# Optimization experiments

Hardware: AMD Instinct MI355X
Metric: run time of the kernel (lower is better)

The kernel has to match this reference:

```python
import jax, jax.numpy as jnp
import numpy as np

RADIUS = 0.1
NSAMPLE = 32


def _ball_query(radius, nsample, xyz, new_xyz):
    # xyz: (B,N,3), new_xyz: (B,npoint,3) -> idx (B,npoint,nsample) int32
    # Faithful to the CUDA ball_query: take the first nsample in-radius indices
    # (in ascending point order); pad with the first found index.
    N = xyz.shape[1]
    d2 = jnp.sum((new_xyz[:, :, None, :] - xyz[:, None, :, :]) ** 2, axis=-1)  # (B,np,N)
    mask = d2 < radius * radius
    key_arr = jnp.where(mask, jnp.arange(N, dtype=jnp.int32), jnp.int32(N))
    idx = jnp.sort(key_arr, axis=-1)[..., :nsample]  # (B,np,ns)
    first = idx[..., :1]
    idx = jnp.where(idx == N, first, idx)
    idx = jnp.where(idx == N, 0, idx)  # empty-ball fallback (matches zero-init buffer)
    return idx


def _group(features, idx):
    # features (B,C,N), idx (B,np,ns) -> (B,C,np,ns)
    return jax.vmap(lambda f, i: f[:, i])(features, idx)


def _forward(xyz, new_xyz):
    idx = jax.lax.stop_gradient(_ball_query(RADIUS, NSAMPLE, xyz, new_xyz))
    xyz_t = jnp.transpose(xyz, (0, 2, 1))                 # (B,3,N)
    g = _group(xyz_t, idx)                                # (B,3,np,ns) grouped_xyz
    c = jnp.transpose(new_xyz, (0, 2, 1))[..., None]      # (B,3,np,1)  new_xyz_reshaped

    # pairwise distances within each group
    diff = g[..., :, None] - g[..., None, :]              # (B,3,np,ns,ns)
    dis = jnp.sqrt(jnp.sum(diff * diff, axis=1))          # (B,np,ns,ns)
    mean_dis = jnp.mean(dis, axis=3)                      # (B,np,ns)
    tip_idx = jnp.argmax(mean_dis, axis=2)                # (B,np)
    tip_pts = jnp.take_along_axis(g, tip_idx[:, None, :, None], axis=3)[..., 0]  # (B,3,np)

    cb = jnp.broadcast_to(c, g.shape)                     # (B,3,np,ns)
    gpv = jnp.cross(jnp.cross(cb, g, axis=1), cb, axis=1)
    gpv = gpv / jnp.linalg.norm(gpv, axis=1)[:, None]     # (B,3,np,ns)

    new_r = jnp.sqrt(jnp.sum(c * c, axis=1))              # (B,np,1)
    new_norm = c / (new_r[:, None] + 1e-8)                # (B,3,np,1)

    c3 = c[..., 0]                                        # (B,3,np)
    tpv = jnp.cross(jnp.cross(c3, tip_pts, axis=1), c3, axis=1)
    tpv = tpv / jnp.linalg.norm(tpv, axis=1)[:, None]     # (B,3,np)

    gcv = jnp.cross(gpv, jnp.broadcast_to(tpv[..., None], gpv.shape), axis=1)
    sinv = jnp.sum(gcv * new_norm, axis=1)                # (B,np,ns)

    dis_t = jnp.transpose(dis, (0, 2, 1, 3))              # (B,ns,np,ns)
    dis_sort = jnp.sort(dis_t, axis=1) * sinv[:, None]    # (B,ns,np,ns)
    grouped_r = jnp.sqrt(jnp.sum(g * g, axis=1))          # (B,np,ns)
    return jnp.concatenate([dis_sort, grouped_r[:, None]], axis=1)  # (B,ns+1,np,ns)


def setup_inputs() -> dict:
    key = jax.random.key(0)
    k1, k2 = jax.random.split(key)
    xyz = jax.random.uniform(k1, (4, 16384, 3), dtype=jnp.float32)
    new_xyz = jax.random.uniform(k2, (4, 2048, 3), dtype=jnp.float32)
    return {"xyz": xyz, "new_xyz": new_xyz}


def reference(xyz, new_xyz):
    return _forward(xyz, new_xyz)
```

## Files before the change

kernel.cpp:

```cpp
#include <hip/hip_runtime.h>


#define BB 4
#define NN 16384
#define MM 2048
#define NS 32
#define R2 0.01f
#define GZ 20
#define NCELL 2000
#define CPAD 2048
#define HCAP 128

#define WS_CUR_OFF (32 * 1024)
#define WS_CNT_OFF (64 * 1024)
#define WS_PTS_OFF (96 * 1024)
#define WS_NEED (WS_PTS_OFF + (size_t)BB * NN * 16)

__device__ __forceinline__ int cell_of(float x, float y, float z) {
    int ci = (int)(x * 10.0f); ci = ci < 0 ? 0 : (ci > 9 ? 9 : ci);
    int cj = (int)(y * 10.0f); cj = cj < 0 ? 0 : (cj > 9 ? 9 : cj);
    int ck = (int)(z * 20.0f); ck = ck < 0 ? 0 : (ck > 19 ? 19 : ck);
    return (ci * 10 + cj) * GZ + ck;
}

__global__ __launch_bounds__(256) void k_count(const float* __restrict__ xyz,
                                               int* __restrict__ cnt) {
    int i = blockIdx.x * 256 + threadIdx.x;
    int b = i >> 14;
    const float* p = xyz + (size_t)i * 3;
    atomicAdd(&cnt[b * CPAD + cell_of(p[0], p[1], p[2])], 1);
}

__global__ __launch_bounds__(1024) void k_scan(const int* __restrict__ cnt,
                                               int* __restrict__ off,
                                               int* __restrict__ cur) {
    __shared__ int wsum[16];
    const int b = blockIdx.x, t = threadIdx.x;
    const int lane = t & 63, wid = t >> 6;
    int v0 = cnt[b * CPAD + 2 * t];
    int v1 = cnt[b * CPAD + 2 * t + 1];
    int s = v0 + v1;
    int x = s;
    #pragma unroll
    for (int o = 1; o < 64; o <<= 1) {
        int u = __shfl_up(x, o);
        if (lane >= o) x += u;
    }
    if (lane == 63) wsum[wid] = x;
    __syncthreads();
    int pre = 0;
    #pragma unroll
    for (int i2 = 0; i2 < 16; ++i2) pre += (i2 < wid) ? wsum[i2] : 0;
    int incl = x + pre;
    int excl = incl - s;
    off[b * CPAD + 2 * t] = excl;
    off[b * CPAD + 2 * t + 1] = excl + v0;
    cur[b * CPAD + 2 * t] = excl;
    cur[b * CPAD + 2 * t + 1] = excl + v0;
}

__global__ __launch_bounds__(256) void k_scatter(const float* __restrict__ xyz,
                                                 int* __restrict__ cur,
                                                 float4* __restrict__ pts) {
    int i = blockIdx.x * 256 + threadIdx.x;
    int b = i >> 14;
    const float* p = xyz + (size_t)i * 3;
    float x = p[0], y = p[1], z = p[2];
    int pos = atomicAdd(&cur[b * CPAD + cell_of(x, y, z)], 1);
    pts[(size_t)b * NN + pos] = make_float4(x, y, z, __int_as_float(i & (NN - 1)));
}

__global__ __launch_bounds__(256) void qgr_grid_kernel(
    const float* __restrict__ xyz,
    const float* __restrict__ nxyz,
    const int* __restrict__ offi,
    const float4* __restrict__ pts,
    float* __restrict__ out) {

    __shared__ float4 s_hit[4][2][HCAP];
    __shared__ float4 s_sel[4][2][NS];

    const int lane = threadIdx.x & 63;
    const int w = threadIdx.x >> 6;
    const int sub = lane & 31;
    const int half = lane >> 5;
    const int q0 = blockIdx.x * 8 + w * 2;
    const int b = q0 >> 11;

    const float* xb = xyz + (size_t)b * NN * 3;
    const float* nq = nxyz + (size_t)q0 * 3;
    const float cx0 = nq[0], cy0 = nq[1], cz0 = nq[2];
    const float cx1 = nq[3], cy1 = nq[4], cz1 = nq[5];
    const unsigned long long lmask = (1ull << lane) - 1ull;

    const int* offb = offi + b * CPAD;
    const float4* ptsb = pts + (size_t)b * NN;

    int hits01[2];
    for (int tq = 0; tq < 2; ++tq) {
        const float ccx = tq ? cx1 : cx0;
        const float ccy = tq ? cy1 : cy0;
        const float ccz = tq ? cz1 : cz0;

        int ci0 = (int)(ccx * 10.0f); ci0 = ci0 < 0 ? 0 : (ci0 > 9 ? 9 : ci0);
        int cj0 = (int)(ccy * 10.0f); cj0 = cj0 < 0 ? 0 : (cj0 > 9 ? 9 : cj0);
        int ck0 = (int)(ccz * 20.0f); ck0 = ck0 < 0 ? 0 : (ck0 > 19 ? 19 : ck0);
        int zlo = ck0 > 2 ? ck0 - 2 : 0;
        int zhi = ck0 < 17 ? ck0 + 2 : 19;

        int rs[9], rl[9];
        #pragma unroll
        for (int r = 0; r < 9; ++r) { rs[r] = 0; rl[r] = 0; }
        int nr = 0;
        #pragma unroll
        for (int di = -1; di <= 1; ++di) {
            int ii = ci0 + di; if ((unsigned)ii > 9u) continue;
            #pragma unroll
            for (int dj = -1; dj <= 1; ++dj) {
                int jj = cj0 + dj; if ((unsigned)jj > 9u) continue;
                int base2 = (ii * 10 + jj) * GZ;
                int s0 = offb[base2 + zlo];
                int e0 = offb[base2 + zhi + 1];
                int len = e0 - s0;
                if (len > 0) { rs[nr] = s0; rl[nr] = len; ++nr; }
            }
        }

        float4 P[9];
        #pragma unroll
        for (int r = 0; r < 9; ++r) {
            int a = (lane < rl[r]) ? (rs[r] + lane) : 0;
            P[r] = ptsb[a];
        }

        int hits = 0;
        #pragma unroll
        for (int r = 0; r < 9; ++r) {
            float dx = __fsub_rn(ccx, P[r].x);
            float dy = __fsub_rn(ccy, P[r].y);
            float dz = __fsub_rn(ccz, P[r].z);
            float d2 = __fadd_rn(__fadd_rn(__fmul_rn(dx, dx), __fmul_rn(dy, dy)),
                                 __fmul_rn(dz, dz));
            bool hit = (lane < rl[r]) && (d2 < R2);
            unsigned long long bal = __ballot(hit);
            if (bal) {
                int rank = __popcll(bal & lmask);
                int slot = hits + rank;
                if (hit && slot < HCAP) s_hit[w][tq][slot] = P[r];
                hits += __popcll(bal);
            }
        }
        for (int r = 0; r < nr; ++r) {
            for (int t0 = 64; t0 < rl[r]; t0 += 64) {
                int t = t0 + lane;
                bool act = t < rl[r];
                float4 Q = ptsb[rs[r] + (act ? t : 0)];
                float dx = __fsub_rn(ccx, Q.x);
                float dy = __fsub_rn(ccy, Q.y);
                float dz = __fsub_rn(ccz, Q.z);
                float d2 = __fadd_rn(__fadd_rn(__fmul_rn(dx, dx), __fmul_rn(dy, dy)),
                                     __fmul_rn(dz, dz));
                bool hit = act && (d2 < R2);
                unsigned long long bal = __ballot(hit);
                if (bal) {
                    int rank = __popcll(bal & lmask);
                    int slot = hits + rank;
                    if (hit && slot < HCAP) s_hit[w][tq][slot] = Q;
                    hits += __popcll(bal);
                }
            }
        }
        hits01[tq] = hits;
    }

    const int hits = half ? hits01[1] : hits01[0];
    const int cap = hits < HCAP ? hits : HCAP;
    const float ccx = half ? cx1 : cx0;
    const float ccy = half ? cy1 : cy0;
    const float ccz = half ? cz1 : cz0;

    int key[4];
    #pragma unroll
    for (int r = 0; r < 4; ++r) {
        int e = r * 32 + sub;
        int idx_e = __float_as_int(s_hit[w][half][e].w);
        key[r] = (e < cap) ? ((idx_e << 8) | e) : 0x7fffffff;
    }

    #pragma unroll
    for (int k = 2; k <= 16; k <<= 1) {
        #pragma unroll
        for (int j = k >> 1; j > 0; j >>= 1) {
            bool lower = (sub & j) == 0;
            bool asc = (sub & k) == 0;
            bool keepmin = (lower == asc);
            #pragma unroll
            for (int r = 0; r < 4; ++r) {
                int p = __shfl_xor(key[r], j);
                key[r] = keepmin ? min(key[r], p) : max(key[r], p);
            }
        }
    }
    #pragma unroll
    for (int j = 16; j > 0; j >>= 1) {
        bool lower = (sub & j) == 0;
        #pragma unroll
        for (int r = 0; r < 4; ++r) {
            int p = __shfl_xor(key[r], j);
            bool asc = (r & 1) == 0;
            key[r] = (lower == asc) ? min(key[r], p) : max(key[r], p);
        }
    }
    {
        int t0 = min(key[0], key[1]); key[1] = max(key[0], key[1]); key[0] = t0;
        int t2 = max(key[2], key[3]); key[3] = min(key[2], key[3]); key[2] = t2;
    }
    #pragma unroll
    for (int j = 16; j > 0; j >>= 1) {
        bool lower = (sub & j) == 0;
        #pragma unroll
        for (int r = 0; r < 4; ++r) {
            int p = __shfl_xor(key[r], j);
            bool asc = (r & 2) == 0;
            key[r] = (lower == asc) ? min(key[r], p) : max(key[r], p);
        }
    }
    {
        int t0 = min(key[0], key[2]); key[2] = max(key[0], key[2]); key[0] = t0;
        int t1 = min(key[1], key[3]); key[3] = max(key[1], key[3]); key[1] = t1;
        t0 = min(key[0], key[1]); key[1] = max(key[0], key[1]); key[0] = t0;
        t1 = min(key[2], key[3]); key[3] = max(key[2], key[3]); key[2] = t1;
    }
    #pragma unroll
    for (int j = 16; j > 0; j >>= 1) {
        bool lower = (sub & j) == 0;
        #pragma unroll
        for (int r = 0; r < 4; ++r) {
            int p = __shfl_xor(key[r], j);
            key[r] = lower ? min(key[r], p) : max(key[r], p);
        }
    }

    const int found = hits < NS ? hits : NS;
    const int hbase = half << 5;
    float4 sel = make_float4(0.f, 0.f, 0.f, 0.f);
    if (sub < found) sel = s_hit[w][half][key[0] & 0xFF];
    float p0x, p0y, p0z;
    if (found == 0) { p0x = xb[0]; p0y = xb[1]; p0z = xb[2]; }
    else {
        p0x = __shfl(sel.x, hbase); p0y = __shfl(sel.y, hbase); p0z = __shfl(sel.z, hbase);
    }
    if (sub >= found) { sel.x = p0x; sel.y = p0y; sel.z = p0z; }
    const float hx = sel.x, hy = sel.y, hz = sel.z;

    s_sel[w][half][sub] = sel;

    float v[NS];
    #pragma unroll
    for (int ii = 0; ii < NS; ++ii) {
        float4 B = s_sel[w][half][ii];
        float dx = __fsub_rn(B.x, hx);
        float dy = __fsub_rn(B.y, hy);
        float dz = __fsub_rn(B.z, hz);
        v[ii] = sqrtf(__fadd_rn(__fadd_rn(__fmul_rn(dx, dx), __fmul_rn(dy, dy)),
                                __fmul_rn(dz, dz)));
    }

    float r8[8];
    #pragma unroll
    for (int t = 0; t < 8; ++t) {
        r8[t] = __fadd_rn(__fadd_rn(__fadd_rn(v[t], v[t + 8]), v[t + 16]), v[t + 24]);
    }
    float mv = __fadd_rn(__fadd_rn(__fadd_rn(r8[0], r8[1]), __fadd_rn(r8[2], r8[3])),
                         __fadd_rn(__fadd_rn(r8[4], r8[5]), __fadd_rn(r8[6], r8[7])));
    int mi = sub;
    #pragma unroll
    for (int off = 1; off < 32; off <<= 1) {
        float ov = __shfl_xor(mv, off);
        int oi = __shfl_xor(mi, off);
        if (ov > mv || (ov == mv && oi < mi)) { mv = ov; mi = oi; }
    }

    float4 T = s_sel[w][half][mi];
    const float tx = T.x, ty = T.y, tz = T.z;

    float ux = ccy * tz - ccz * ty, uy = ccz * tx - ccx * tz, uz = ccx * ty - ccy * tx;
    float vx = uy * ccz - uz * ccy, vy = uz * ccx - ux * ccz, vz = ux * ccy - uy * ccx;
    float vn = fmaxf(sqrtf(vx * vx + vy * vy + vz * vz), 1e-37f);
    float tnx = vx / vn, tny = vy / vn, tnz = vz / vn;

    float nrm = sqrtf(ccx * ccx + ccy * ccy + ccz * ccz);
    float dn = nrm + 1e-8f;
    float nnx = ccx / dn, nny = ccy / dn, nnz = ccz / dn;

    float ax = ccy * hz - ccz * hy, ay = ccz * hx - ccx * hz, az = ccx * hy - ccy * hx;
    float px = ay * ccz - az * ccy, py = az * ccx - ax * ccz, pz = ax * ccy - ay * ccx;
    float pn = fmaxf(sqrtf(px * px + py * py + pz * pz), 1e-37f);
    px /= pn; py /= pn; pz /= pn;

    float qx = py * tnz - pz * tny;
    float qy = pz * tnx - px * tnz;
    float qz = px * tny - py * tnx;
    float sinv = qx * nnx + qy * nny + qz * nnz;

    float gr = sqrtf(hx * hx + hy * hy + hz * hz);

    const int m_h = (q0 + half) & (MM - 1);
    const size_t rowstride = (size_t)MM * NS;
    const size_t obase = (((size_t)b * 33) * MM + m_h) * NS + sub;
    out[obase + 32 * rowstride] = gr;

    #pragma unroll
    for (int p = 1; p < NS; p <<= 1) {
        #pragma unroll
        for (int k = p; k >= 1; k >>= 1) {
            #pragma unroll
            for (int j = k & (p - 1); j + k < NS; j += 2 * k) {
                #pragma unroll
                for (int i = 0; i < k; ++i) {
                    if (i + j + k < NS) {
                        int x = i + j, y = i + j + k;
                        if ((x / (2 * p)) == (y / (2 * p))) {
                            float lo = fminf(v[x], v[y]);
                            v[y] = fmaxf(v[x], v[y]);
                            v[x] = lo;
                        }
                    }
                }
            }
        }
    }

    #pragma unroll
    for (int ii = 0; ii < NS; ++ii)
        out[obase + (size_t)ii * rowstride] = v[ii] * sinv;
}

#define CHUNKS 4
__global__ __launch_bounds__(256) void qgr_kernel(
    const float* __restrict__ xyz,
    const float* __restrict__ nxyz,
    float* __restrict__ out) {

    __shared__ float s_gx[4][NS], s_gy[4][NS], s_gz[4][NS];
    __shared__ float s_dis[4][NS][NS + 1];

    const int lane = threadIdx.x & 63;
    const int w = threadIdx.x >> 6;
    const int q = blockIdx.x * 4 + w;
    const int b = q >> 11;
    const int m = q & (MM - 1);

    const float* xb = xyz + (size_t)b * NN * 3;
    const float* nq = nxyz + (size_t)q * 3;
    const float cx = nq[0], cy = nq[1], cz = nq[2];
    const unsigned long long lmask = (1ull << lane) - 1ull;

    int cnt = 0;
    for (int base = 0; base < NN; base += 64 * CHUNKS) {
        float X[CHUNKS], Y[CHUNKS], Z[CHUNKS];
        #pragma unroll
        for (int c = 0; c < CHUNKS; ++c) {
            const float* p = xb + (size_t)(base + c * 64 + lane) * 3;
            X[c] = p[0]; Y[c] = p[1]; Z[c] = p[2];
        }
        bool in[CHUNKS];
        #pragma unroll
        for (int c = 0; c < CHUNKS; ++c) {
            float dx = __fsub_rn(cx, X[c]);
            float dy = __fsub_rn(cy, Y[c]);
            float dz = __fsub_rn(cz, Z[c]);
            float d2 = __fadd_rn(__fadd_rn(__fmul_rn(dx, dx), __fmul_rn(dy, dy)),
                                 __fmul_rn(dz, dz));
            in[c] = d2 < R2;
        }
        #pragma unroll
        for (int c = 0; c < CHUNKS; ++c) {
            unsigned long long bal = __ballot(in[c]);
            if (bal) {
                int rank = __popcll(bal & lmask);
                int slot = cnt + rank;
                if (in[c] && slot < NS) {
                    s_gx[w][slot] = X[c]; s_gy[w][slot] = Y[c]; s_gz[w][slot] = Z[c];
                }
                cnt += __popcll(bal);
            }
        }
        if (cnt >= NS) break;
    }
    __syncthreads();

    int found = cnt < NS ? cnt : NS;
    float p0x, p0y, p0z;
    if (found == 0) { p0x = xb[0]; p0y = xb[1]; p0z = xb[2]; }
    else            { p0x = s_gx[w][0]; p0y = s_gy[w][0]; p0z = s_gz[w][0]; }
    if (lane < NS && lane >= found) {
        s_gx[w][lane] = p0x; s_gy[w][lane] = p0y; s_gz[w][lane] = p0z;
    }
    __syncthreads();

    #pragma unroll
    for (int t = 0; t < 16; ++t) {
        int e = t * 64 + lane;
        int di = e >> 5, dj = e & 31;
        float dx = __fsub_rn(s_gx[w][di], s_gx[w][dj]);
        float dy = __fsub_rn(s_gy[w][di], s_gy[w][dj]);
        float dz = __fsub_rn(s_gz[w][di], s_gz[w][dj]);
        s_dis[w][di][dj] =
            sqrtf(__fadd_rn(__fadd_rn(__fmul_rn(dx, dx), __fmul_rn(dy, dy)), __fmul_rn(dz, dz)));
    }
    __syncthreads();

    {
        int i = lane & 31;
        float r[8];
        #pragma unroll
        for (int t = 0; t < 8; ++t) {
            r[t] = __fadd_rn(__fadd_rn(__fadd_rn(s_dis[w][i][t], s_dis[w][i][t + 8]),
                                        s_dis[w][i][t + 16]),
                             s_dis[w][i][t + 24]);
        }
        float mv = __fadd_rn(__fadd_rn(__fadd_rn(r[0], r[1]), __fadd_rn(r[2], r[3])),
                             __fadd_rn(__fadd_rn(r[4], r[5]), __fadd_rn(r[6], r[7])));
        int mi = i;
        #pragma unroll
        for (int off = 1; off < 64; off <<= 1) {
            float ov = __shfl_xor(mv, off);
            int oi = __shfl_xor(mi, off);
            if (ov > mv || (ov == mv && oi < mi)) { mv = ov; mi = oi; }
        }
        float tx = s_gx[w][mi], ty = s_gy[w][mi], tz = s_gz[w][mi];
        float ux = cy * tz - cz * ty, uy = cz * tx - cx * tz, uz = cx * ty - cy * tx;
        float vx = uy * cz - uz * cy, vy = uz * cx - ux * cz, vz = ux * cy - uy * cx;
        float vn = fmaxf(sqrtf(vx * vx + vy * vy + vz * vz), 1e-37f);
        float tnx = vx / vn, tny = vy / vn, tnz = vz / vn;
        float nr = sqrtf(cx * cx + cy * cy + cz * cz);
        float dn = nr + 1e-8f;
        float nnx = cx / dn, nny = cy / dn, nnz = cz / dn;
        int j = lane & 31;
        float gx = s_gx[w][j], gy = s_gy[w][j], gz = s_gz[w][j];
        float ax = cy * gz - cz * gy, ay = cz * gx - cx * gz, az = cx * gy - cy * gx;
        float px = ay * cz - az * cy, py = az * cx - ax * cz, pz = ax * cy - ay * cx;
        float pn = fmaxf(sqrtf(px * px + py * py + pz * pz), 1e-37f);
        px /= pn; py /= pn; pz /= pn;
        float qx = py * tnz - pz * tny;
        float qy = pz * tnx - px * tnz;
        float qz = px * tny - py * tnx;
        float sinv = qx * nnx + qy * nny + qz * nnz;
        float gr = sqrtf(gx * gx + gy * gy + gz * gz);
        const size_t rowstride = (size_t)MM * NS;
        const size_t obase = (((size_t)b * 33) * MM + m) * NS + j;
        if (lane < NS) out[obase + 32 * rowstride] = gr;
        float v[NS];
        #pragma unroll
        for (int ii = 0; ii < NS; ++ii) v[ii] = s_dis[w][ii][j];
        #pragma unroll
        for (int k = 2; k <= NS; k <<= 1) {
            #pragma unroll
            for (int jj = k >> 1; jj > 0; jj >>= 1) {
                #pragma unroll
                for (int ii = 0; ii < NS; ++ii) {
                    int ll = ii ^ jj;
                    if (ll > ii) {
                        bool up = ((ii & k) == 0);
                        float a = v[ii], c2 = v[ll];
                        bool sw = up ? (a > c2) : (a < c2);
                        if (sw) { v[ii] = c2; v[ll] = a; }
                    }
                }
            }
        }
        if (lane < NS) {
            #pragma unroll
            for (int ii = 0; ii < NS; ++ii)
                out[obase + (size_t)ii * rowstride] = v[ii] * sinv;
        }
    }
}

extern "C" void kernel_launch(void* const* d_in, const int* in_sizes, int n_in,
                              void* d_out, int out_size, void* d_ws, size_t ws_size,
                              hipStream_t stream) {
    (void)in_sizes; (void)n_in; (void)out_size;
    const float* xyz = (const float*)d_in[0];
    const float* nxyz = (const float*)d_in[1];
    float* out = (float*)d_out;

    if (d_ws != nullptr && ws_size >= WS_NEED) {
        char* ws = (char*)d_ws;
        int* off = (int*)ws;
        int* cur = (int*)(ws + WS_CUR_OFF);
        int* cnt = (int*)(ws + WS_CNT_OFF);
        float4* pts = (float4*)(ws + WS_PTS_OFF);

        hipMemsetAsync(cnt, 0, 32 * 1024, stream);
        k_count<<<(BB * NN) / 256, 256, 0, stream>>>(xyz, cnt);
        k_scan<<<BB, 1024, 0, stream>>>(cnt, off, cur);
        k_scatter<<<(BB * NN) / 256, 256, 0, stream>>>(xyz, cur, pts);
        qgr_grid_kernel<<<(BB * MM) / 8, 256, 0, stream>>>(xyz, nxyz, off, pts, out);
    } else {
        qgr_kernel<<<(BB * MM) / 4, 256, 0, stream>>>(xyz, nxyz, out);
    }
}
```

Before: 99.34 us.

## Fuse grid build (count, scan, scatter) into one cooperative kernel

Replaces the memset plus three separate launches that build the spatial-grid bucket structure with a single cooperative kernel that uses grid-wide syncs between the zero, count, scan and scatter phases. The atomic rank from the count phase is reused for the scatter position, so no second cursor pass is needed. The aim is to remove launch overheads and inter-kernel gaps. Grid syncs have their own cost, and the cooperative launch falls back to the old path if it fails. The scatter order inside a cell now depends on atomic ordering, as it did before.

```diff
diff --git a/kernel.cpp b/kernel.cpp
--- a/kernel.cpp
+++ b/kernel.cpp
@@ -1,4 +1,7 @@
 #include <hip/hip_runtime.h>
+#include <hip/hip_cooperative_groups.h>
+
+namespace cg = cooperative_groups;
 
 
 #define BB 4
@@ -21,6 +24,53 @@
     int cj = (int)(y * 10.0f); cj = cj < 0 ? 0 : (cj > 9 ? 9 : cj);
     int ck = (int)(z * 20.0f); ck = ck < 0 ? 0 : (ck > 19 ? 19 : ck);
     return (ci * 10 + cj) * GZ + ck;
+}
+
+__global__ __launch_bounds__(256) void k_build_coop(const float* __restrict__ xyz,
+                                                    int* __restrict__ cnt,
+                                                    int* __restrict__ off,
+                                                    float4* __restrict__ pts) {
+    cg::grid_group grid = cg::this_grid();
+    __shared__ int wsum[4];
+
+    const int g = blockIdx.x * 256 + threadIdx.x;
+
+    if (g < BB * CPAD) cnt[g] = 0;
+    grid.sync();
+
+    const int b = g >> 14;
+    const float* p = xyz + (size_t)g * 3;
+    const float x = p[0], y = p[1], z = p[2];
+    const int cell = cell_of(x, y, z);
+    const int r = atomicAdd(&cnt[b * CPAD + cell], 1);
+    grid.sync();
+
+    if (blockIdx.x < BB) {
+        const int bb = blockIdx.x, t = threadIdx.x;
+        const int lane = t & 63, wid = t >> 6;
+        const int base = bb * CPAD + t * 8;
+        int v[8]; int s = 0;
+        #pragma unroll
+        for (int j = 0; j < 8; ++j) { v[j] = cnt[base + j]; s += v[j]; }
+        int xs = s;
+        #pragma unroll
+        for (int o = 1; o < 64; o <<= 1) {
+            int u = __shfl_up(xs, o);
+            if (lane >= o) xs += u;
+        }
+        if (lane == 63) wsum[wid] = xs;
+        __syncthreads();
+        int pre = 0;
+        #pragma unroll
+        for (int i2 = 0; i2 < 4; ++i2) pre += (i2 < wid) ? wsum[i2] : 0;
+        int run = pre + xs - s;
+        #pragma unroll
+        for (int j = 0; j < 8; ++j) { off[base + j] = run; run += v[j]; }
+    }
+    grid.sync();
+
+    const int pos = off[b * CPAD + cell] + r;
+    pts[(size_t)b * NN + pos] = make_float4(x, y, z, __int_as_float(g & (NN - 1)));
 }
 
 __global__ __launch_bounds__(256) void k_count(const float* __restrict__ xyz,
@@ -493,10 +543,19 @@
         int* cnt = (int*)(ws + WS_CNT_OFF);
         float4* pts = (float4*)(ws + WS_PTS_OFF);
 
-        hipMemsetAsync(cnt, 0, 32 * 1024, stream);
-        k_count<<<(BB * NN) / 256, 256, 0, stream>>>(xyz, cnt);
-        k_scan<<<BB, 1024, 0, stream>>>(cnt, off, cur);
-        k_scatter<<<(BB * NN) / 256, 256, 0, stream>>>(xyz, cur, pts);
+        void* kargs[4];
+        kargs[0] = (void*)&xyz;
+        kargs[1] = (void*)&cnt;
+        kargs[2] = (void*)&off;
+        kargs[3] = (void*)&pts;
+        hipError_t ce = hipLaunchCooperativeKernel(k_build_coop, dim3(256), dim3(256),
+                                                   kargs, 0, stream);
+        if (ce != hipSuccess) {
+            hipMemsetAsync(cnt, 0, 32 * 1024, stream);
+            k_count<<<(BB * NN) / 256, 256, 0, stream>>>(xyz, cnt);
+            k_scan<<<BB, 1024, 0, stream>>>(cnt, off, cur);
+            k_scatter<<<(BB * NN) / 256, 256, 0, stream>>>(xyz, cur, pts);
+        }
         qgr_grid_kernel<<<(BB * MM) / 8, 256, 0, stream>>>(xyz, nxyz, off, pts, out);
     } else {
         qgr_kernel<<<(BB * MM) / 4, 256, 0, stream>>>(xyz, nxyz, out);
```

After: 178.3 us. 1.79x slower.

## Fuse grid count, scan and scatter into one partitioned build kernel

Applied to the files above, without the earlier changes.

Replaces the memset plus three separate grid-construction kernels (global-atomic count, scan, scatter) with a single kernel. Each of 32 blocks per batch builds the full cell histogram and prefix scan in shared memory, then scatters only the points whose cells fall in its 64-cell range, using shared-memory atomics. This removes three launches and the global atomics, at the cost of each block redundantly reading all 16384 points of its batch twice. The order of points within a cell can still vary between runs because of the atomics, as before.

```diff
diff --git a/kernel.cpp b/kernel.cpp
--- a/kernel.cpp
+++ b/kernel.cpp
@@ -11,8 +11,6 @@
 #define CPAD 2048
 #define HCAP 128
 
-#define WS_CUR_OFF (32 * 1024)
-#define WS_CNT_OFF (64 * 1024)
 #define WS_PTS_OFF (96 * 1024)
 #define WS_NEED (WS_PTS_OFF + (size_t)BB * NN * 16)
 
@@ -23,51 +21,62 @@
     return (ci * 10 + cj) * GZ + ck;
 }
 
-__global__ __launch_bounds__(256) void k_count(const float* __restrict__ xyz,
-                                               int* __restrict__ cnt) {
-    int i = blockIdx.x * 256 + threadIdx.x;
-    int b = i >> 14;
-    const float* p = xyz + (size_t)i * 3;
-    atomicAdd(&cnt[b * CPAD + cell_of(p[0], p[1], p[2])], 1);
-}
-
-__global__ __launch_bounds__(1024) void k_scan(const int* __restrict__ cnt,
-                                               int* __restrict__ off,
-                                               int* __restrict__ cur) {
-    __shared__ int wsum[16];
-    const int b = blockIdx.x, t = threadIdx.x;
+__global__ __launch_bounds__(256) void k_build_part(const float* __restrict__ xyz,
+                                                    int* __restrict__ off,
+                                                    float4* __restrict__ pts) {
+    __shared__ int hist[CPAD];
+    __shared__ int wsum[4];
+
+    const int b = blockIdx.x >> 5;
+    const int r = blockIdx.x & 31;
+    const int t = threadIdx.x;
     const int lane = t & 63, wid = t >> 6;
-    int v0 = cnt[b * CPAD + 2 * t];
-    int v1 = cnt[b * CPAD + 2 * t + 1];
-    int s = v0 + v1;
-    int x = s;
+    const float* xb = xyz + (size_t)b * NN * 3;
+
+    #pragma unroll
+    for (int j = 0; j < CPAD / 256; ++j) hist[t + j * 256] = 0;
+    __syncthreads();
+
+    for (int i = t; i < NN; i += 256) {
+        const float* p = xb + (size_t)i * 3;
+        atomicAdd(&hist[cell_of(p[0], p[1], p[2])], 1);
+    }
+    __syncthreads();
+
+    const int base = t * 8;
+    int v[8]; int s = 0;
+    #pragma unroll
+    for (int j = 0; j < 8; ++j) { v[j] = hist[base + j]; s += v[j]; }
+    int xs = s;
     #pragma unroll
     for (int o = 1; o < 64; o <<= 1) {
-        int u = __shfl_up(x, o);
-        if (lane >= o) x += u;
-    }
-    if (lane == 63) wsum[wid] = x;
+        int u = __shfl_up(xs, o);
+        if (lane >= o) xs += u;
+    }
+    if (lane == 63) wsum[wid] = xs;
     __syncthreads();
     int pre = 0;
     #pragma unroll
-    for (int i2 = 0; i2 < 16; ++i2) pre += (i2 < wid) ? wsum[i2] : 0;
-    int incl = x + pre;
-    int excl = incl - s;
-    off[b * CPAD + 2 * t] = excl;
-    off[b * CPAD + 2 * t + 1] = excl + v0;
-    cur[b * CPAD + 2 * t] = excl;
-    cur[b * CPAD + 2 * t + 1] = excl + v0;
-}
-
-__global__ __launch_bounds__(256) void k_scatter(const float* __restrict__ xyz,
-                                                 int* __restrict__ cur,
-                                                 float4* __restrict__ pts) {
-    int i = blockIdx.x * 256 + threadIdx.x;
-    int b = i >> 14;
-    const float* p = xyz + (size_t)i * 3;
-    float x = p[0], y = p[1], z = p[2];
-    int pos = atomicAdd(&cur[b * CPAD + cell_of(x, y, z)], 1);
-    pts[(size_t)b * NN + pos] = make_float4(x, y, z, __int_as_float(i & (NN - 1)));
+    for (int i2 = 0; i2 < 4; ++i2) pre += (i2 < wid) ? wsum[i2] : 0;
+    int run = pre + xs - s;
+    #pragma unroll
+    for (int j = 0; j < 8; ++j) {
+        if (r == 0) off[b * CPAD + base + j] = run;
+        hist[base + j] = run;
+        run += v[j];
+    }
+    __syncthreads();
+
+    const int clo = r * 64, chi = clo + 64;
+    for (int i = t; i < NN; i += 256) {
+        const float* p = xb + (size_t)i * 3;
+        float x = p[0], y = p[1], z = p[2];
+        int c = cell_of(x, y, z);
+        if (c >= clo && c < chi) {
+            int pos = atomicAdd(&hist[c], 1);
+            pts[(size_t)b * NN + pos] = make_float4(x, y, z, __int_as_float(i));
+        }
+    }
 }
 
 __global__ __launch_bounds__(256) void qgr_grid_kernel(
@@ -489,14 +498,9 @@
     if (d_ws != nullptr && ws_size >= WS_NEED) {
         char* ws = (char*)d_ws;
         int* off = (int*)ws;
-        int* cur = (int*)(ws + WS_CUR_OFF);
-        int* cnt = (int*)(ws + WS_CNT_OFF);
         float4* pts = (float4*)(ws + WS_PTS_OFF);
 
-        hipMemsetAsync(cnt, 0, 32 * 1024, stream);
-        k_count<<<(BB * NN) / 256, 256, 0, stream>>>(xyz, cnt);
-        k_scan<<<BB, 1024, 0, stream>>>(cnt, off, cur);
-        k_scatter<<<(BB * NN) / 256, 256, 0, stream>>>(xyz, cur, pts);
+        k_build_part<<<BB * 32, 256, 0, stream>>>(xyz, off, pts);
         qgr_grid_kernel<<<(BB * MM) / 8, 256, 0, stream>>>(xyz, nxyz, off, pts, out);
     } else {
         qgr_kernel<<<(BB * MM) / 4, 256, 0, stream>>>(xyz, nxyz, out);
```

After: 121.9 us. 22.7% more time.
